# Kernel optimization log

Hardware: AMD Instinct MI355X
Metric: run time of the kernel (lower is better)

Reference implementation:

```python
import jax, jax.numpy as jnp
import numpy as np

NUM_REGIONS = 3
REGION_SIZE = 384
IMG_SIZE = 512
PEAK_WINDOW = 5


def setup_inputs() -> dict:
    key = jax.random.key(0)
    ks = jax.random.split(key, 6)
    B, C, Hf, Wf = 32, 1024, 32, 32
    features = jax.random.normal(ks[0], (B, C, Hf, Wf), jnp.float32)
    cam_32x32 = jax.random.uniform(ks[1], (B, 32, 32), jnp.float32)
    original = jax.random.normal(ks[2], (B, 3, IMG_SIZE, IMG_SIZE), jnp.float32)
    def init_w(k, o, i):
        return jax.random.normal(k, (o, i), jnp.float32) * (1.0 / np.sqrt(i).astype(np.float32))
    w1 = init_w(ks[3], 512, C); b1 = jnp.zeros((512,), jnp.float32)
    w2 = init_w(ks[4], 256, 512); b2 = jnp.zeros((256,), jnp.float32)
    w3 = init_w(ks[5], 1, 256); b3 = jnp.zeros((1,), jnp.float32)
    return dict(features=features, cam_32x32=cam_32x32, original=original,
                w1=w1, b1=b1, w2=w2, b2=b2, w3=w3, b3=b3)


def _attention(features, w1, b1, w2, b2, w3, b3):
    # stack of 1x1 convs == per-pixel matmuls
    h = jax.nn.relu(jnp.einsum('bchw,oc->bohw', features, w1) + b1[None, :, None, None])
    h = jax.nn.relu(jnp.einsum('bchw,oc->bohw', h, w2) + b2[None, :, None, None])
    return jax.nn.sigmoid(jnp.einsum('bchw,oc->bohw', h, w3) + b3[None, :, None, None])


def _pick_peaks(score_map, K):
    # iterative argmax + square-window suppression (NMS-style peak picking)
    Hf, Wf = score_map.shape
    ys = jnp.arange(Hf)[:, None]
    xs = jnp.arange(Wf)[None, :]
    def step(scores, _):
        flat = jnp.argmax(scores)
        val = scores.reshape(-1)[flat]
        fy = (flat // Wf).astype(jnp.int32)
        fx = (flat % Wf).astype(jnp.int32)
        valid = val > 0.0
        fy = jnp.where(valid, fy, Hf // 2).astype(jnp.int32)
        fx = jnp.where(valid, fx, Wf // 2).astype(jnp.int32)
        supp = (jnp.abs(ys - fy) <= PEAK_WINDOW) & (jnp.abs(xs - fx) <= PEAK_WINDOW)
        return jnp.where(supp, jnp.zeros_like(scores), scores), jnp.stack([fy, fx])
    _, peaks = jax.lax.scan(step, score_map, None, length=K)
    return peaks  # [K, 2] (fy, fx)


def reference(features, cam_32x32, original, w1, b1, w2, b2, w3, b3):
    B, C, Hf, Wf = features.shape
    att = _attention(features, w1, b1, w2, b2, w3, b3)  # [B,1,Hf,Wf]
    # bilinear (align_corners=False) resize of CAM to feature grid
    cam_f = jax.image.resize(cam_32x32[:, None], (B, 1, Hf, Wf), 'bilinear')
    att = (att + cam_f) * 0.5

    peaks = jax.vmap(lambda m: _pick_peaks(m, NUM_REGIONS))(att[:, 0])  # [B,K,2]
    sy = IMG_SIZE / float(Hf)
    sx = IMG_SIZE / float(Wf)
    cy = jnp.floor(peaks[..., 0].astype(jnp.float32) * sy).astype(jnp.int32)
    cx = jnp.floor(peaks[..., 1].astype(jnp.float32) * sx).astype(jnp.int32)
    half = REGION_SIZE // 2
    # clamp-and-adjust logic collapses to a clip when img >= region size
    y1 = jnp.clip(cy - half, 0, IMG_SIZE - REGION_SIZE)
    x1 = jnp.clip(cx - half, 0, IMG_SIZE - REGION_SIZE)

    Cimg = original.shape[1]
    def crop_img(img, y1s, x1s):
        return jax.vmap(lambda y, x: jax.lax.dynamic_slice(
            img, (0, y, x), (Cimg, REGION_SIZE, REGION_SIZE)))(y1s, x1s)
    regions = jax.vmap(crop_img)(original, y1, x1)  # [B,K,3,rs,rs]
    regions = regions.reshape(B * NUM_REGIONS, Cimg, REGION_SIZE, REGION_SIZE)
    coords = jnp.stack([x1, y1, x1 + REGION_SIZE, y1 + REGION_SIZE], axis=-1)  # [B,K,4]
    return regions, coords, att
```

## Files before the change

kernel.cpp:

```cpp
#include <hip/hip_runtime.h>
#include <cstdint>
#include <cmath>


typedef float f4 __attribute__((ext_vector_type(4)));
typedef _Float16 f16x8 __attribute__((ext_vector_type(8)));
typedef int i4 __attribute__((ext_vector_type(4)));
typedef unsigned short u16x4 __attribute__((ext_vector_type(4)));

#define M_PIX 32768
#define COORDS_OFF 42467328
#define ATT_OFF 42467712

#define FHI_OFF 0
#define FLO_OFF 8388608
#define H2_OFF 0
#define H1HI_OFF 16777216
#define H1LO_OFF 25165824
#define W1HI_OFF 33554432
#define W1LO_OFF 33816576
#define W2HI_OFF 34078720
#define W2LO_OFF 34144256

#define GLOAD16(gp, lp) \
    __builtin_amdgcn_global_load_lds( \
        (const __attribute__((address_space(1))) unsigned int*)(gp), \
        (__attribute__((address_space(3))) unsigned int*)(lp), 16, 0, 0)

__device__ __forceinline__ int swz(int row, int k16) {
    return ((row << 4) + (k16 >> 1)) ^ ((row & 7) << 2);
}

__device__ __forceinline__ int split_pack(float v0, float v1, int& lop) {
    _Float16 h0 = (_Float16)v0, h1 = (_Float16)v1;
    float r0 = v0 - (float)h0, r1 = v1 - (float)h1;
    _Float16 l0 = (_Float16)r0, l1 = (_Float16)r1;
    unsigned int uh0 = __builtin_bit_cast(unsigned short, h0);
    unsigned int uh1 = __builtin_bit_cast(unsigned short, h1);
    unsigned int ul0 = __builtin_bit_cast(unsigned short, l0);
    unsigned int ul1 = __builtin_bit_cast(unsigned short, l1);
    lop = (int)(ul0 | (ul1 << 16));
    return (int)(uh0 | (uh1 << 16));
}

__global__ __launch_bounds__(256) void split_plane(
    const float* __restrict__ src, unsigned short* __restrict__ hi,
    unsigned short* __restrict__ lo, int n4)
{
    const int i = blockIdx.x * 256 + threadIdx.x;
    if (i >= n4) return;
    f4 v = *(const f4*)(src + 4 * (size_t)i);
    u16x4 hv, lv;
    #pragma unroll
    for (int j = 0; j < 4; ++j) {
        _Float16 h = (_Float16)v[j];
        _Float16 l = (_Float16)(v[j] - (float)h);
        hv[j] = __builtin_bit_cast(unsigned short, h);
        lv[j] = __builtin_bit_cast(unsigned short, l);
    }
    *(u16x4*)(hi + 4 * (size_t)i) = hv;
    *(u16x4*)(lo + 4 * (size_t)i) = lv;
}

__global__ __launch_bounds__(256) void split_tile_f(
    const float* __restrict__ feat, unsigned int* __restrict__ fhi,
    unsigned int* __restrict__ flo, int pb_base)
{
    const int blk = blockIdx.x;
    const int lpb = blk >> 5, kb = blk & 31;
    const int pb  = pb_base + lpb;
    const int t = threadIdx.x;
    __shared__ float ftile[32][128];

    const int k   = t >> 3;
    const int pxl = (t & 7) * 16;
    const int px0 = pb * 128;
    const size_t base = ((size_t)(px0 >> 10) << 20)
                      + (size_t)(kb * 32 + k) * 1024 + (px0 & 1023) + pxl;
    #pragma unroll
    for (int j = 0; j < 4; ++j)
        *(f4*)&ftile[k][pxl + 4 * j] = *(const f4*)(feat + base + 4 * j);
    __syncthreads();

    const int L   = 8 * t;
    const int rL  = L >> 4;
    const int row = rL ^ ((rL >> 2) & 1);
    const int cb  = L & 15;
    unsigned int hp[8], lp[8];
    #pragma unroll
    for (int j = 0; j < 8; ++j) {
        const int kint = (cb + j) ^ ((row & 3) << 2);
        int lo;
        int hi = split_pack(ftile[2 * kint][row], ftile[2 * kint + 1][row], lo);
        hp[j] = (unsigned int)hi; lp[j] = (unsigned int)lo;
    }
    unsigned int* oh = fhi + (((size_t)lpb * 32 + kb) << 11) + L;
    unsigned int* ol = flo + (((size_t)lpb * 32 + kb) << 11) + L;
    *(i4*)(oh)     = *(i4*)&hp[0];
    *(i4*)(oh + 4) = *(i4*)&hp[4];
    *(i4*)(ol)     = *(i4*)&lp[0];
    *(i4*)(ol + 4) = *(i4*)&lp[4];
}

template<int MODE, int NBL, int NKB>
__global__ __launch_bounds__(256, 2) void gemm_mfma(
    const unsigned short* __restrict__ WH, const unsigned short* __restrict__ WL,
    const unsigned int* __restrict__ FH, const unsigned int* __restrict__ FL,
    const float* __restrict__ bias, void* __restrict__ OA, void* __restrict__ OB,
    int pb_base)
{
    constexpr int Kdim = NKB * 32;
    __shared__ int lds[16384];

    const int t = threadIdx.x;
    const int lane = t & 63;
    const int wave = t >> 6;
    const int wn = wave >> 1, wp = wave & 1;

    const int f   = blockIdx.x;
    const int nb  = (f >> 3) & ((1 << NBL) - 1);
    const int lpb = (f & 7) | ((f >> (3 + NBL)) << 3);
    const int n0  = nb * 128;
    const int px0 = (pb_base + lpb) * 128;

    int wg_off[2];
    #pragma unroll
    for (int j = 0; j < 2; ++j) {
        const int i  = 2 * wave + j;
        const int rL = 16 * i + (lane >> 2);
        const int r  = rL ^ ((rL >> 2) & 1);
        const int c  = (4 * (lane & 3)) ^ ((r & 3) << 2);
        wg_off[j] = (n0 + r) * Kdim + 2 * c;
    }

    const unsigned int* fhb = FH + ((size_t)lpb * NKB << 11) + 256 * (2 * wave) + 4 * lane;
    const unsigned int* flb = FL + ((size_t)lpb * NKB << 11) + 256 * (2 * wave) + 4 * lane;

    f4 acc[4][4];
    #pragma unroll
    for (int i = 0; i < 4; ++i)
        #pragma unroll
        for (int j = 0; j < 4; ++j) acc[i][j] = (f4){0.f, 0.f, 0.f, 0.f};

    auto DMA = [&](int buf, int kb) {
        const int wb = buf * 4096, fb = 8192 + buf * 4096;
        const int k0 = kb * 32;
        #pragma unroll
        for (int j = 0; j < 2; ++j) {
            const int i = 2 * wave + j;
            GLOAD16(WH + wg_off[j] + k0, &lds[wb + 256 * i]);
            GLOAD16(WL + wg_off[j] + k0, &lds[wb + 2048 + 256 * i]);
            GLOAD16(fhb + ((size_t)kb << 11) + 256 * j, &lds[fb + 256 * i]);
            GLOAD16(flb + ((size_t)kb << 11) + 256 * j, &lds[fb + 2048 + 256 * i]);
        }
    };

    const int rA0 = 64 * wn + (lane & 15);
    const int rB0 = 64 * wp + (lane & 15);
    const int kg  = (lane >> 4) * 8;

    DMA(0, 0);
    int cur = 0;
    for (int kb = 0; kb < NKB; ++kb) {
        __syncthreads();
        if (kb + 1 < NKB) DMA(cur ^ 1, kb + 1);

        const int wb = cur * 4096, fb = 8192 + cur * 4096;
        f16x8 bh[4], bl[4];
        #pragma unroll
        for (int nf = 0; nf < 4; ++nf) {
            bh[nf] = *(const f16x8*)&lds[fb + swz(rB0 + 16 * nf, kg)];
            bl[nf] = *(const f16x8*)&lds[fb + 2048 + swz(rB0 + 16 * nf, kg)];
        }
        #pragma unroll
        for (int m = 0; m < 4; ++m) {
            f16x8 ah = *(const f16x8*)&lds[wb + swz(rA0 + 16 * m, kg)];
            f16x8 al = *(const f16x8*)&lds[wb + 2048 + swz(rA0 + 16 * m, kg)];
            #pragma unroll
            for (int nf = 0; nf < 4; ++nf) {
                acc[m][nf] = __builtin_amdgcn_mfma_f32_16x16x32_f16(ah, bh[nf], acc[m][nf], 0, 0, 0);
                acc[m][nf] = __builtin_amdgcn_mfma_f32_16x16x32_f16(ah, bl[nf], acc[m][nf], 0, 0, 0);
                acc[m][nf] = __builtin_amdgcn_mfma_f32_16x16x32_f16(al, bh[nf], acc[m][nf], 0, 0, 0);
            }
        }
        cur ^= 1;
    }

    if constexpr (MODE == 0) {
        __syncthreads();
        #pragma unroll
        for (int m = 0; m < 4; ++m) {
            const int n_l = 64 * wn + 4 * (lane >> 4) + 16 * m;
            const f4 bv = *(const f4*)&bias[n0 + n_l];
            const int kb_l = n_l >> 5;
            #pragma unroll
            for (int nf = 0; nf < 4; ++nf) {
                const int row = 64 * wp + (lane & 15) + 16 * nf;
                float v0 = fmaxf(acc[m][nf][0] + bv[0], 0.0f);
                float v1 = fmaxf(acc[m][nf][1] + bv[1], 0.0f);
                float v2 = fmaxf(acc[m][nf][2] + bv[2], 0.0f);
                float v3 = fmaxf(acc[m][nf][3] + bv[3], 0.0f);
                int lo0, lo1;
                int hi0 = split_pack(v0, v1, lo0);
                int hi1 = split_pack(v2, v3, lo1);
                const int i0 = swz(row, (n_l & 31));
                const int i1 = swz(row, (n_l & 31) + 2);
                lds[kb_l * 2048 + i0]        = hi0;
                lds[kb_l * 2048 + i1]        = hi1;
                lds[8192 + kb_l * 2048 + i0] = lo0;
                lds[8192 + kb_l * 2048 + i1] = lo1;
            }
        }
        __syncthreads();
        const int g = t >> 5;
        const int l32 = t & 31;
        const int pb = pb_base + lpb;
        unsigned int* h1hi = (unsigned int*)OA;
        unsigned int* h1lo = (unsigned int*)OB;
        unsigned int* dst = ((g >> 2) ? h1lo : h1hi)
                          + (((size_t)pb * 16 + 4 * nb + (g & 3)) << 11) + 64 * l32;
        const int* src = &lds[(g >> 2) * 8192 + (g & 3) * 2048 + 64 * l32];
        #pragma unroll
        for (int q = 0; q < 16; ++q)
            *(i4*)(dst + 4 * q) = *(const i4*)(src + 4 * q);
    } else {
        float* o32 = (float*)OA;
        const int pxE = px0 + 64 * wp + (lane & 15);
        const int nE  = n0 + 64 * wn + 4 * (lane >> 4);
        #pragma unroll
        for (int m = 0; m < 4; ++m) {
            const int n_m = nE + 16 * m;
            const f4 bv = *(const f4*)&bias[n_m];
            #pragma unroll
            for (int nf = 0; nf < 4; ++nf) {
                const int p = pxE + 16 * nf;
                #pragma unroll
                for (int r = 0; r < 4; ++r)
                    o32[(size_t)(n_m + r) * M_PIX + p] = fmaxf(acc[m][nf][r] + bv[r], 0.0f);
            }
        }
    }
}

__global__ __launch_bounds__(256) void layer3_att(
    const float* __restrict__ h2, const float* __restrict__ w3,
    const float* __restrict__ b3, const float* __restrict__ cam,
    float* __restrict__ att)
{
    const int p = blockIdx.x * 256 + threadIdx.x;
    float s = b3[0];
    #pragma unroll 8
    for (int k = 0; k < 256; ++k)
        s = fmaf(w3[k], h2[(size_t)k * M_PIX + p], s);
    const float sg = 1.0f / (1.0f + expf(-s));
    att[p] = (sg + cam[p]) * 0.5f;
}

__global__ __launch_bounds__(64) void peaks_kernel(
    const float* __restrict__ att, float* __restrict__ coords,
    int* __restrict__ wsyx)
{
    const int b = blockIdx.x;
    const int lane = threadIdx.x;
    __shared__ float s[1024];
    for (int i = lane; i < 1024; i += 64) s[i] = att[b * 1024 + i];
    __syncthreads();

    for (int kpk = 0; kpk < 3; ++kpk) {
        float bv = -1.0f;
        int bi = 0x7fffffff;
        for (int i = lane; i < 1024; i += 64) {
            float v = s[i];
            if (v > bv) { bv = v; bi = i; }
        }
        for (int off = 32; off >= 1; off >>= 1) {
            float ov = __shfl_down(bv, off);
            int   oi = __shfl_down(bi, off);
            if (ov > bv || (ov == bv && oi < bi)) { bv = ov; bi = oi; }
        }
        bv = __shfl(bv, 0);
        bi = __shfl(bi, 0);

        int fy, fx;
        if (bv > 0.0f) { fy = bi >> 5; fx = bi & 31; }
        else           { fy = 16;      fx = 16; }

        for (int i = lane; i < 1024; i += 64) {
            const int y = i >> 5, x = i & 31;
            const int dy = y > fy ? y - fy : fy - y;
            const int dx = x > fx ? x - fx : fx - x;
            if (dy <= 5 && dx <= 5) s[i] = 0.0f;
        }
        __syncthreads();

        if (lane == 0) {
            int y1 = fy * 16 - 192; y1 = y1 < 0 ? 0 : (y1 > 128 ? 128 : y1);
            int x1 = fx * 16 - 192; x1 = x1 < 0 ? 0 : (x1 > 128 ? 128 : x1);
            const int idx = b * 3 + kpk;
            coords[idx * 4 + 0] = (float)x1;
            coords[idx * 4 + 1] = (float)y1;
            coords[idx * 4 + 2] = (float)(x1 + 384);
            coords[idx * 4 + 3] = (float)(y1 + 384);
            wsyx[idx * 2 + 0] = y1;
            wsyx[idx * 2 + 1] = x1;
        }
        __syncthreads();
    }
}

__global__ __launch_bounds__(256) void crop_kernel(
    const float* __restrict__ orig, const int* __restrict__ wsyx,
    float* __restrict__ out)
{
    const int id = blockIdx.x * 256 + threadIdx.x;
    const int r    = id / (3 * 384 * 96);
    const int rem  = id - r * (3 * 384 * 96);
    const int c    = rem / (384 * 96);
    const int rem2 = rem - c * (384 * 96);
    const int row  = rem2 / 96;
    const int col  = (rem2 - row * 96) * 4;
    const int b = r / 3;
    const int y1 = wsyx[r * 2], x1 = wsyx[r * 2 + 1];
    const float* src = orig + (size_t)b * 786432 + (size_t)c * 262144
                     + (size_t)(y1 + row) * 512 + x1 + col;
    *(f4*)(out + (size_t)id * 4) = *(const f4*)src;
}

extern "C" void kernel_launch(void* const* d_in, const int* in_sizes, int n_in,
                              void* d_out, int out_size, void* d_ws, size_t ws_size,
                              hipStream_t stream)
{
    const float* features = (const float*)d_in[0];
    const float* cam      = (const float*)d_in[1];
    const float* original = (const float*)d_in[2];
    const float* w1 = (const float*)d_in[3];
    const float* b1 = (const float*)d_in[4];
    const float* w2 = (const float*)d_in[5];
    const float* b2 = (const float*)d_in[6];
    const float* w3 = (const float*)d_in[7];
    const float* b3 = (const float*)d_in[8];

    float* out = (float*)d_out;
    unsigned int* fhi  = (unsigned int*)(out + FHI_OFF);
    unsigned int* flo  = (unsigned int*)(out + FLO_OFF);
    unsigned int* h1hi = (unsigned int*)(out + H1HI_OFF);
    unsigned int* h1lo = (unsigned int*)(out + H1LO_OFF);
    float* h2 = out + H2_OFF;
    unsigned short* w1hi = (unsigned short*)(out + W1HI_OFF);
    unsigned short* w1lo = (unsigned short*)(out + W1LO_OFF);
    unsigned short* w2hi = (unsigned short*)(out + W2HI_OFF);
    unsigned short* w2lo = (unsigned short*)(out + W2LO_OFF);
    float* att    = out + ATT_OFF;
    float* coords = out + COORDS_OFF;
    int*   wsyx   = (int*)d_ws;

    dim3 b256(256);
    split_plane<<<dim3(512), b256, 0, stream>>>(w1, w1hi, w1lo, 131072);
    split_plane<<<dim3(128), b256, 0, stream>>>(w2, w2hi, w2lo, 32768);
    split_tile_f<<<dim3(4096), b256, 0, stream>>>(features, fhi, flo, 0);
    gemm_mfma<0, 2, 32><<<dim3(512), b256, 0, stream>>>(
        w1hi, w1lo, fhi, flo, b1, h1hi, h1lo, 0);
    split_tile_f<<<dim3(4096), b256, 0, stream>>>(features, fhi, flo, 128);
    gemm_mfma<0, 2, 32><<<dim3(512), b256, 0, stream>>>(
        w1hi, w1lo, fhi, flo, b1, h1hi, h1lo, 128);
    gemm_mfma<1, 1, 16><<<dim3(512), b256, 0, stream>>>(
        w2hi, w2lo, h1hi, h1lo, b2, h2, nullptr, 0);
    layer3_att<<<dim3(128), b256, 0, stream>>>(h2, w3, b3, cam, att);
    peaks_kernel<<<dim3(32), dim3(64), 0, stream>>>(att, coords, wsyx);
    crop_kernel<<<dim3(41472), b256, 0, stream>>>(original, wsyx, out);
}
```

Measured before the change: 513.1 us.

## Fuse fp32 feature hi/lo split into layer-1 GEMM, drop split_tile_f pre-pass

New measurement: 451.3 us. 12.1% less time.

```diff
diff --git a/kernel.cpp b/kernel.cpp
--- a/kernel.cpp
+++ b/kernel.cpp
@@ -12,15 +12,13 @@
 #define COORDS_OFF 42467328
 #define ATT_OFF 42467712
 
-#define FHI_OFF 0
-#define FLO_OFF 8388608
-#define H2_OFF 0
-#define H1HI_OFF 16777216
-#define H1LO_OFF 25165824
-#define W1HI_OFF 33554432
-#define W1LO_OFF 33816576
-#define W2HI_OFF 34078720
-#define W2LO_OFF 34144256
+#define H1HI_OFF 0
+#define H1LO_OFF 8388608
+#define H2_OFF 16777216
+#define W1HI_OFF 25165824
+#define W1LO_OFF 25427968
+#define W2HI_OFF 25690112
+#define W2LO_OFF 25755648
 
 #define GLOAD16(gp, lp) \
     __builtin_amdgcn_global_load_lds( \
@@ -62,54 +60,12 @@
     *(u16x4*)(lo + 4 * (size_t)i) = lv;
 }
 
-__global__ __launch_bounds__(256) void split_tile_f(
-    const float* __restrict__ feat, unsigned int* __restrict__ fhi,
-    unsigned int* __restrict__ flo, int pb_base)
-{
-    const int blk = blockIdx.x;
-    const int lpb = blk >> 5, kb = blk & 31;
-    const int pb  = pb_base + lpb;
-    const int t = threadIdx.x;
-    __shared__ float ftile[32][128];
-
-    const int k   = t >> 3;
-    const int pxl = (t & 7) * 16;
-    const int px0 = pb * 128;
-    const size_t base = ((size_t)(px0 >> 10) << 20)
-                      + (size_t)(kb * 32 + k) * 1024 + (px0 & 1023) + pxl;
-    #pragma unroll
-    for (int j = 0; j < 4; ++j)
-        *(f4*)&ftile[k][pxl + 4 * j] = *(const f4*)(feat + base + 4 * j);
-    __syncthreads();
-
-    const int L   = 8 * t;
-    const int rL  = L >> 4;
-    const int row = rL ^ ((rL >> 2) & 1);
-    const int cb  = L & 15;
-    unsigned int hp[8], lp[8];
-    #pragma unroll
-    for (int j = 0; j < 8; ++j) {
-        const int kint = (cb + j) ^ ((row & 3) << 2);
-        int lo;
-        int hi = split_pack(ftile[2 * kint][row], ftile[2 * kint + 1][row], lo);
-        hp[j] = (unsigned int)hi; lp[j] = (unsigned int)lo;
-    }
-    unsigned int* oh = fhi + (((size_t)lpb * 32 + kb) << 11) + L;
-    unsigned int* ol = flo + (((size_t)lpb * 32 + kb) << 11) + L;
-    *(i4*)(oh)     = *(i4*)&hp[0];
-    *(i4*)(oh + 4) = *(i4*)&hp[4];
-    *(i4*)(ol)     = *(i4*)&lp[0];
-    *(i4*)(ol + 4) = *(i4*)&lp[4];
-}
-
-template<int MODE, int NBL, int NKB>
-__global__ __launch_bounds__(256, 2) void gemm_mfma(
+__global__ __launch_bounds__(256, 2) void gemm_k1(
     const unsigned short* __restrict__ WH, const unsigned short* __restrict__ WL,
-    const unsigned int* __restrict__ FH, const unsigned int* __restrict__ FL,
-    const float* __restrict__ bias, void* __restrict__ OA, void* __restrict__ OB,
-    int pb_base)
-{
-    constexpr int Kdim = NKB * 32;
+    const float* __restrict__ feat, const float* __restrict__ bias,
+    unsigned int* __restrict__ OHI, unsigned int* __restrict__ OLO)
+{
+    constexpr int Kdim = 1024;
     __shared__ int lds[16384];
 
     const int t = threadIdx.x;
@@ -117,11 +73,16 @@
     const int wave = t >> 6;
     const int wn = wave >> 1, wp = wave & 1;
 
-    const int f   = blockIdx.x;
-    const int nb  = (f >> 3) & ((1 << NBL) - 1);
-    const int lpb = (f & 7) | ((f >> (3 + NBL)) << 3);
+    const int f  = blockIdx.x;
+    const int nb = (f >> 3) & 3;
+    const int pb = (f & 7) | ((f >> 5) << 3);
     const int n0  = nb * 128;
-    const int px0 = (pb_base + lpb) * 128;
+    const int px0 = pb * 128;
+
+    const int rl = t & 127;
+    const int kb = (t >> 7) * 16;
+
+    const float* F32 = feat + ((size_t)(px0 >> 10) << 20) + (px0 & 1023) + rl;
 
     int wg_off[2];
     #pragma unroll
@@ -133,25 +94,40 @@
         wg_off[j] = (n0 + r) * Kdim + 2 * c;
     }
 
-    const unsigned int* fhb = FH + ((size_t)lpb * NKB << 11) + 256 * (2 * wave) + 4 * lane;
-    const unsigned int* flb = FL + ((size_t)lpb * NKB << 11) + 256 * (2 * wave) + 4 * lane;
-
     f4 acc[4][4];
     #pragma unroll
     for (int i = 0; i < 4; ++i)
         #pragma unroll
         for (int j = 0; j < 4; ++j) acc[i][j] = (f4){0.f, 0.f, 0.f, 0.f};
 
-    auto DMA = [&](int buf, int kb) {
-        const int wb = buf * 4096, fb = 8192 + buf * 4096;
-        const int k0 = kb * 32;
+    float fv[16];
+
+    auto W_GLOADS = [&](int buf, int k0) {
+        const int wb = buf * 4096;
         #pragma unroll
         for (int j = 0; j < 2; ++j) {
             const int i = 2 * wave + j;
             GLOAD16(WH + wg_off[j] + k0, &lds[wb + 256 * i]);
             GLOAD16(WL + wg_off[j] + k0, &lds[wb + 2048 + 256 * i]);
-            GLOAD16(fhb + ((size_t)kb << 11) + 256 * j, &lds[fb + 256 * i]);
-            GLOAD16(flb + ((size_t)kb << 11) + 256 * j, &lds[fb + 2048 + 256 * i]);
+        }
+    };
+    auto LOADS_F = [&](int k0) {
+        #pragma unroll
+        for (int j = 0; j < 16; ++j)
+            fv[j] = F32[(size_t)(k0 + kb + j) * 1024];
+    };
+    auto STAGE_F = [&]() {
+        #pragma unroll
+        for (int g = 0; g < 2; ++g) {
+            i4 hp, lp;
+            #pragma unroll
+            for (int j = 0; j < 4; ++j) {
+                int lo;
+                hp[j] = split_pack(fv[8 * g + 2 * j], fv[8 * g + 2 * j + 1], lo);
+                lp[j] = lo;
+            }
+            *(i4*)&lds[8192  + swz(rl, kb + 8 * g)] = hp;
+            *(i4*)&lds[10240 + swz(rl, kb + 8 * g)] = lp;
         }
     };
 
@@ -159,18 +135,20 @@
     const int rB0 = 64 * wp + (lane & 15);
     const int kg  = (lane >> 4) * 8;
 
-    DMA(0, 0);
+    W_GLOADS(0, 0);
+    LOADS_F(0);
     int cur = 0;
-    for (int kb = 0; kb < NKB; ++kb) {
+    for (int k0 = 0; k0 < Kdim; k0 += 32) {
+        STAGE_F();
         __syncthreads();
-        if (kb + 1 < NKB) DMA(cur ^ 1, kb + 1);
-
-        const int wb = cur * 4096, fb = 8192 + cur * 4096;
+        if (k0 + 32 < Kdim) { W_GLOADS(cur ^ 1, k0 + 32); LOADS_F(k0 + 32); }
+
+        const int wb = cur * 4096;
         f16x8 bh[4], bl[4];
         #pragma unroll
         for (int nf = 0; nf < 4; ++nf) {
-            bh[nf] = *(const f16x8*)&lds[fb + swz(rB0 + 16 * nf, kg)];
-            bl[nf] = *(const f16x8*)&lds[fb + 2048 + swz(rB0 + 16 * nf, kg)];
+            bh[nf] = *(const f16x8*)&lds[8192  + swz(rB0 + 16 * nf, kg)];
+            bl[nf] = *(const f16x8*)&lds[10240 + swz(rB0 + 16 * nf, kg)];
         }
         #pragma unroll
         for (int m = 0; m < 4; ++m) {
@@ -183,61 +161,139 @@
                 acc[m][nf] = __builtin_amdgcn_mfma_f32_16x16x32_f16(al, bh[nf], acc[m][nf], 0, 0, 0);
             }
         }
+        __syncthreads();
         cur ^= 1;
     }
 
-    if constexpr (MODE == 0) {
+    #pragma unroll
+    for (int m = 0; m < 4; ++m) {
+        const int n_l = 64 * wn + 4 * (lane >> 4) + 16 * m;
+        const f4 bv = *(const f4*)&bias[n0 + n_l];
+        const int kb_l = n_l >> 5;
+        #pragma unroll
+        for (int nf = 0; nf < 4; ++nf) {
+            const int row = 64 * wp + (lane & 15) + 16 * nf;
+            float v0 = fmaxf(acc[m][nf][0] + bv[0], 0.0f);
+            float v1 = fmaxf(acc[m][nf][1] + bv[1], 0.0f);
+            float v2 = fmaxf(acc[m][nf][2] + bv[2], 0.0f);
+            float v3 = fmaxf(acc[m][nf][3] + bv[3], 0.0f);
+            int lo0, lo1;
+            int hi0 = split_pack(v0, v1, lo0);
+            int hi1 = split_pack(v2, v3, lo1);
+            const int i0 = swz(row, (n_l & 31));
+            const int i1 = swz(row, (n_l & 31) + 2);
+            lds[kb_l * 2048 + i0]        = hi0;
+            lds[kb_l * 2048 + i1]        = hi1;
+            lds[8192 + kb_l * 2048 + i0] = lo0;
+            lds[8192 + kb_l * 2048 + i1] = lo1;
+        }
+    }
+    __syncthreads();
+    const int g = t >> 5;
+    const int l32 = t & 31;
+    unsigned int* dst = ((g >> 2) ? OLO : OHI)
+                      + (((size_t)pb * 16 + 4 * nb + (g & 3)) << 11);
+    const int* src = &lds[(g >> 2) * 8192 + (g & 3) * 2048];
+    #pragma unroll
+    for (int q = 0; q < 16; ++q)
+        *(i4*)(dst + 128 * q + 4 * l32) = *(const i4*)(src + 128 * q + 4 * l32);
+}
+
+__global__ __launch_bounds__(256, 2) void gemm_k2(
+    const unsigned short* __restrict__ WH, const unsigned short* __restrict__ WL,
+    const unsigned int* __restrict__ FH, const unsigned int* __restrict__ FL,
+    const float* __restrict__ bias, float* __restrict__ OUT)
+{
+    constexpr int NKB = 16;
+    constexpr int Kdim = NKB * 32;
+    __shared__ int lds[16384];
+
+    const int t = threadIdx.x;
+    const int lane = t & 63;
+    const int wave = t >> 6;
+    const int wn = wave >> 1, wp = wave & 1;
+
+    const int f   = blockIdx.x;
+    const int nb  = (f >> 3) & 1;
+    const int lpb = (f & 7) | ((f >> 4) << 3);
+    const int n0  = nb * 128;
+    const int px0 = lpb * 128;
+
+    int wg_off[2];
+    #pragma unroll
+    for (int j = 0; j < 2; ++j) {
+        const int i  = 2 * wave + j;
+        const int rL = 16 * i + (lane >> 2);
+        const int r  = rL ^ ((rL >> 2) & 1);
+        const int c  = (4 * (lane & 3)) ^ ((r & 3) << 2);
+        wg_off[j] = (n0 + r) * Kdim + 2 * c;
+    }
+
+    const unsigned int* fhb = FH + ((size_t)lpb * NKB << 11) + 256 * (2 * wave) + 4 * lane;
+    const unsigned int* flb = FL + ((size_t)lpb * NKB << 11) + 256 * (2 * wave) + 4 * lane;
+
+    f4 acc[4][4];
+    #pragma unroll
+    for (int i = 0; i < 4; ++i)
+        #pragma unroll
+        for (int j = 0; j < 4; ++j) acc[i][j] = (f4){0.f, 0.f, 0.f, 0.f};
+
+    auto DMA = [&](int buf, int kbi) {
+        const int wb = buf * 4096, fb = 8192 + buf * 4096;
+        const int k0 = kbi * 32;
+        #pragma unroll
+        for (int j = 0; j < 2; ++j) {
+            const int i = 2 * wave + j;
+            GLOAD16(WH + wg_off[j] + k0, &lds[wb + 256 * i]);
+            GLOAD16(WL + wg_off[j] + k0, &lds[wb + 2048 + 256 * i]);
+            GLOAD16(fhb + ((size_t)kbi << 11) + 256 * j, &lds[fb + 256 * i]);
+            GLOAD16(flb + ((size_t)kbi << 11) + 256 * j, &lds[fb + 2048 + 256 * i]);
+        }
+    };
+
+    const int rA0 = 64 * wn + (lane & 15);
+    const int rB0 = 64 * wp + (lane & 15);
+    const int kg  = (lane >> 4) * 8;
+
+    DMA(0, 0);
+    int cur = 0;
+    for (int kbi = 0; kbi < NKB; ++kbi) {
         __syncthreads();
+        if (kbi + 1 < NKB) DMA(cur ^ 1, kbi + 1);
+
+        const int wb = cur * 4096, fb = 8192 + cur * 4096;
+        f16x8 bh[4], bl[4];
+        #pragma unroll
+        for (int nf = 0; nf < 4; ++nf) {
+            bh[nf] = *(const f16x8*)&lds[fb + swz(rB0 + 16 * nf, kg)];
+            bl[nf] = *(const f16x8*)&lds[fb + 2048 + swz(rB0 + 16 * nf, kg)];
+        }
         #pragma unroll
         for (int m = 0; m < 4; ++m) {
-            const int n_l = 64 * wn + 4 * (lane >> 4) + 16 * m;
-            const f4 bv = *(const f4*)&bias[n0 + n_l];
-            const int kb_l = n_l >> 5;
+            f16x8 ah = *(const f16x8*)&lds[wb + swz(rA0 + 16 * m, kg)];
+            f16x8 al = *(const f16x8*)&lds[wb + 2048 + swz(rA0 + 16 * m, kg)];
             #pragma unroll
             for (int nf = 0; nf < 4; ++nf) {
-                const int row = 64 * wp + (lane & 15) + 16 * nf;
-                float v0 = fmaxf(acc[m][nf][0] + bv[0], 0.0f);
-                float v1 = fmaxf(acc[m][nf][1] + bv[1], 0.0f);
-                float v2 = fmaxf(acc[m][nf][2] + bv[2], 0.0f);
-                float v3 = fmaxf(acc[m][nf][3] + bv[3], 0.0f);
-                int lo0, lo1;
-                int hi0 = split_pack(v0, v1, lo0);
-                int hi1 = split_pack(v2, v3, lo1);
-                const int i0 = swz(row, (n_l & 31));
-                const int i1 = swz(row, (n_l & 31) + 2);
-                lds[kb_l * 2048 + i0]        = hi0;
-                lds[kb_l * 2048 + i1]        = hi1;
-                lds[8192 + kb_l * 2048 + i0] = lo0;
-                lds[8192 + kb_l * 2048 + i1] = lo1;
+                acc[m][nf] = __builtin_amdgcn_mfma_f32_16x16x32_f16(ah, bh[nf], acc[m][nf], 0, 0, 0);
+                acc[m][nf] = __builtin_amdgcn_mfma_f32_16x16x32_f16(ah, bl[nf], acc[m][nf], 0, 0, 0);
+                acc[m][nf] = __builtin_amdgcn_mfma_f32_16x16x32_f16(al, bh[nf], acc[m][nf], 0, 0, 0);
             }
         }
-        __syncthreads();
-        const int g = t >> 5;
-        const int l32 = t & 31;
-        const int pb = pb_base + lpb;
-        unsigned int* h1hi = (unsigned int*)OA;
-        unsigned int* h1lo = (unsigned int*)OB;
-        unsigned int* dst = ((g >> 2) ? h1lo : h1hi)
-                          + (((size_t)pb * 16 + 4 * nb + (g & 3)) << 11) + 64 * l32;
-        const int* src = &lds[(g >> 2) * 8192 + (g & 3) * 2048 + 64 * l32];
-        #pragma unroll
-        for (int q = 0; q < 16; ++q)
-            *(i4*)(dst + 4 * q) = *(const i4*)(src + 4 * q);
-    } else {
-        float* o32 = (float*)OA;
-        const int pxE = px0 + 64 * wp + (lane & 15);
-        const int nE  = n0 + 64 * wn + 4 * (lane >> 4);
-        #pragma unroll
-        for (int m = 0; m < 4; ++m) {
-            const int n_m = nE + 16 * m;
-            const f4 bv = *(const f4*)&bias[n_m];
+        cur ^= 1;
+    }
+
+    const int pxE = px0 + 64 * wp + (lane & 15);
+    const int nE  = n0 + 64 * wn + 4 * (lane >> 4);
+    #pragma unroll
+    for (int m = 0; m < 4; ++m) {
+        const int n_m = nE + 16 * m;
+        const f4 bv = *(const f4*)&bias[n_m];
+        #pragma unroll
+        for (int nf = 0; nf < 4; ++nf) {
+            const int p = pxE + 16 * nf;
             #pragma unroll
-            for (int nf = 0; nf < 4; ++nf) {
-                const int p = pxE + 16 * nf;
-                #pragma unroll
-                for (int r = 0; r < 4; ++r)
-                    o32[(size_t)(n_m + r) * M_PIX + p] = fmaxf(acc[m][nf][r] + bv[r], 0.0f);
-            }
+            for (int r = 0; r < 4; ++r)
+                OUT[(size_t)(n_m + r) * M_PIX + p] = fmaxf(acc[m][nf][r] + bv[r], 0.0f);
         }
     }
 }
@@ -341,8 +397,6 @@
     const float* b3 = (const float*)d_in[8];
 
     float* out = (float*)d_out;
-    unsigned int* fhi  = (unsigned int*)(out + FHI_OFF);
-    unsigned int* flo  = (unsigned int*)(out + FLO_OFF);
     unsigned int* h1hi = (unsigned int*)(out + H1HI_OFF);
     unsigned int* h1lo = (unsigned int*)(out + H1LO_OFF);
     float* h2 = out + H2_OFF;
@@ -357,14 +411,8 @@
     dim3 b256(256);
     split_plane<<<dim3(512), b256, 0, stream>>>(w1, w1hi, w1lo, 131072);
     split_plane<<<dim3(128), b256, 0, stream>>>(w2, w2hi, w2lo, 32768);
-    split_tile_f<<<dim3(4096), b256, 0, stream>>>(features, fhi, flo, 0);
-    gemm_mfma<0, 2, 32><<<dim3(512), b256, 0, stream>>>(
-        w1hi, w1lo, fhi, flo, b1, h1hi, h1lo, 0);
-    split_tile_f<<<dim3(4096), b256, 0, stream>>>(features, fhi, flo, 128);
-    gemm_mfma<0, 2, 32><<<dim3(512), b256, 0, stream>>>(
-        w1hi, w1lo, fhi, flo, b1, h1hi, h1lo, 128);
-    gemm_mfma<1, 1, 16><<<dim3(512), b256, 0, stream>>>(
-        w2hi, w2lo, h1hi, h1lo, b2, h2, nullptr, 0);
+    gemm_k1<<<dim3(1024), b256, 0, stream>>>(w1hi, w1lo, features, b1, h1hi, h1lo);
+    gemm_k2<<<dim3(512), b256, 0, stream>>>(w2hi, w2lo, h1hi, h1lo, b2, h2);
     layer3_att<<<dim3(128), b256, 0, stream>>>(h2, w3, b3, cam, att);
     peaks_kernel<<<dim3(32), dim3(64), 0, stream>>>(att, coords, wsyx);
     crop_kernel<<<dim3(41472), b256, 0, stream>>>(original, wsyx, out);
```
